# Kernel tuning notes

Hardware: AMD Instinct MI355X
Metric: run time of the kernel (lower is better)

The kernel has to match this reference:

```python
import jax, jax.numpy as jnp
import numpy as np

NUM_HEADS = 16
HEAD_DIM = 128
D = NUM_HEADS * HEAD_DIM  # 2048
B, S = 4, 2048
NEG = jnp.finfo(jnp.float32).min


def setup_inputs() -> dict:
    key = jax.random.key(0)
    ks = jax.random.split(key, 6)
    scale = 1.0 / np.sqrt(D)
    return {
        "hidden_states": jax.random.normal(ks[0], (B, S, D), jnp.float32),
        "wq": jax.random.normal(ks[1], (D, D), jnp.float32) * scale,
        "wk": jax.random.normal(ks[2], (D, D), jnp.float32) * scale,
        "wv": jax.random.normal(ks[3], (D, D), jnp.float32) * scale,
        "wo": jax.random.normal(ks[4], (D, D), jnp.float32) * scale,
        "bo": jnp.zeros((D,), jnp.float32),
    }


def _split_heads(x):
    b, s, _ = x.shape
    return x.reshape(b, s, NUM_HEADS, HEAD_DIM).transpose(0, 2, 1, 3)  # [B,H,S,Dh]


def reference(hidden_states, wq, wk, wv, wo, bo):
    # projections (nn.Linear: x @ W^T), no bias for q/k/v
    q = _split_heads(hidden_states @ wq.T).astype(jnp.float32)
    k = _split_heads(hidden_states @ wk.T).astype(jnp.float32)
    v = _split_heads(hidden_states @ wv.T)
    # GPT-Neo: NO 1/sqrt(d) scaling
    scores = jnp.einsum("bhqd,bhkd->bhqk", q, k)  # [B,H,S,S] fp32
    s = scores.shape[-1]
    causal = jnp.tril(jnp.ones((s, s), bool))  # [S,S]
    scores = jnp.where(causal[None, None], scores, NEG)
    attn_weights = jax.nn.softmax(scores, axis=-1).astype(v.dtype)
    # dropout is identity at eval (p=0.0)
    attn_output = jnp.einsum("bhqk,bhkd->bhqd", attn_weights, v)
    attn_output = attn_output.transpose(0, 2, 1, 3).reshape(hidden_states.shape)
    attn_output = attn_output @ wo.T + bo
    return attn_output, attn_weights
```

## Files before the change

### kernel.cpp

```cpp
#include <hip/hip_runtime.h>

#define DEVFN static __device__ __forceinline__

typedef _Float16 f16;
typedef f16 f16x8 __attribute__((ext_vector_type(8)));
typedef f16 f16x4 __attribute__((ext_vector_type(4)));
typedef float f32x4 __attribute__((ext_vector_type(4)));
typedef short short8 __attribute__((ext_vector_type(8)));

constexpr int Bc = 4, Hn = 16, Sn = 2048, DH = 128, Dn = 2048;
constexpr long MROWS = (long)Bc * Sn;
constexpr long LDQK = 2 * Dn;

template <typename T, typename C>
DEVFN auto mfma_impl(T a, T b, C c, int)
    -> decltype(__builtin_amdgcn_mfma_f32_16x16x32_f16(a, b, c, 0, 0, 0)) {
  return __builtin_amdgcn_mfma_f32_16x16x32_f16(a, b, c, 0, 0, 0);
}
template <typename T, typename C>
DEVFN C mfma_impl(T a, T b, C c, long) {
  return __builtin_amdgcn_mfma_f32_16x16x32_f16(
      __builtin_bit_cast(short8, a), __builtin_bit_cast(short8, b), c, 0, 0, 0);
}
DEVFN f32x4 MFMA(f16x8 a, f16x8 b, f32x4 c) { return mfma_impl(a, b, c, 0); }

DEVFN void nt_store(float* p, float v) { __builtin_nontemporal_store(v, p); }
DEVFN void nt_store4(float* p, f32x4 v) {
  __builtin_nontemporal_store(v, (f32x4*)p);
}

DEVFN void gld_lds16(const f16* g, f16* s) {
  __builtin_amdgcn_global_load_lds(
      (const __attribute__((address_space(1))) unsigned int*)g,
      (__attribute__((address_space(3))) unsigned int*)s, 16, 0, 0);
}

DEVFN void stage_tile(const f16* __restrict__ g, long ld, f16* __restrict__ s) {
  const int t = threadIdx.x;
  const int rr = t >> 3;
  const int cb = (t & 7) * 16;
#pragma unroll
  for (int ch = 0; ch < 4; ++ch) {
    const int r = ch * 32 + rr;
    const int scb = cb ^ ((r & 7) << 4);
    gld_lds16(g + (long)r * ld + (scb >> 1), s + r * 64 + (cb >> 1));
  }
}

DEVFN void stage_tile128(const f16* __restrict__ g, long ld, f16* __restrict__ s) {
  const int t = threadIdx.x;
  const int rr = t >> 4;
  const int cb = (t & 15) * 16;
#pragma unroll
  for (int ch = 0; ch < 8; ++ch) {
    const int r = ch * 16 + rr;
    const int scb = cb ^ ((r & 7) << 4);
    gld_lds16(g + (long)r * ld + (scb >> 1), s + r * 128 + (cb >> 1));
  }
}

DEVFN f16x8 ldfrag(const f16* s, int row, int kelem) {
  const int cb = (kelem * 2) ^ ((row & 7) << 4);
  return *(const f16x8*)(s + row * 64 + (cb >> 1));
}

DEVFN f16x8 ldfrag128(const f16* s, int row, int kelem) {
  const int cb = (kelem * 2) ^ ((row & 7) << 4);
  return *(const f16x8*)((const char*)s + row * 256 + cb);
}

DEVFN f16x8 ldfrag64(const f16* s, int row, int kelem) {
  const int cb = (kelem * 2) ^ ((row & 7) << 4);
  return *(const f16x8*)((const char*)s + row * 128 + cb);
}

__global__ __launch_bounds__(256) void k_cvt_all(
    const float* __restrict__ hid, const float* __restrict__ wq,
    const float* __restrict__ wk, const float* __restrict__ wv,
    const float* __restrict__ wo, f16* __restrict__ h16,
    f16* __restrict__ wqk16, f16* __restrict__ wv16, f16* __restrict__ wo16) {
  const int y = blockIdx.y;
  const long nW = (long)Dn * Dn;
  const float* x;
  f16* out;
  if (y < 4) {
    x = hid + (long)y * nW;
    out = h16 + (long)y * nW;
  } else if (y == 4) {
    x = wq; out = wqk16;
  } else if (y == 5) {
    x = wk; out = wqk16 + nW;
  } else if (y == 6) {
    x = wv; out = wv16;
  } else {
    x = wo; out = wo16;
  }
  const long i = ((long)blockIdx.x * 256 + threadIdx.x) * 4;
  float4 v = *(const float4*)(x + i);
  f16x4 h;
  h[0] = (f16)v.x; h[1] = (f16)v.y; h[2] = (f16)v.z; h[3] = (f16)v.w;
  *(f16x4*)(out + i) = h;
}

DEVFN void gemm_body(const f16* __restrict__ A, long ldA,
                     const f16* __restrict__ B, long ldB, int K,
                     f16* __restrict__ oh, long ldC, int nt, int mt,
                     float oscale, f16* sA, f16* sB) {
  const int tid = threadIdx.x, w = tid >> 6, lane = tid & 63;
  const int wm = (w >> 1) * 64, wn = (w & 1) * 64;
  const int lr = lane & 15, lg = lane >> 4;
  f32x4 acc[4][4] = {};
  const f16* Ab = A + (long)mt * 128 * ldA;
  const f16* Bb = B + (long)nt * 128 * ldB;

  stage_tile(Ab, ldA, sA);
  stage_tile(Bb, ldB, sB);
  __syncthreads();

  int cur = 0;
  for (int kt = 0; kt < K; kt += 64) {
    if (kt + 64 < K) {
      stage_tile(Ab + kt + 64, ldA, sA + (cur ^ 1) * (128 * 64));
      stage_tile(Bb + kt + 64, ldB, sB + (cur ^ 1) * (128 * 64));
    }
    const f16* cA = sA + cur * (128 * 64);
    const f16* cB = sB + cur * (128 * 64);
#pragma unroll
    for (int kk = 0; kk < 64; kk += 32) {
      f16x8 ahf[4], bhf[4];
#pragma unroll
      for (int m = 0; m < 4; ++m) ahf[m] = ldfrag(cA, wm + m * 16 + lr, kk + lg * 8);
#pragma unroll
      for (int n = 0; n < 4; ++n) bhf[n] = ldfrag(cB, wn + n * 16 + lr, kk + lg * 8);
#pragma unroll
      for (int m = 0; m < 4; ++m)
#pragma unroll
        for (int n = 0; n < 4; ++n) acc[m][n] = MFMA(ahf[m], bhf[n], acc[m][n]);
    }
    __syncthreads();
    cur ^= 1;
  }

#pragma unroll
  for (int m = 0; m < 4; ++m)
#pragma unroll
    for (int n = 0; n < 4; ++n) {
      const int col = nt * 128 + wn + n * 16 + lr;
#pragma unroll
      for (int r = 0; r < 4; ++r) {
        const long row = (long)mt * 128 + wm + m * 16 + lg * 4 + r;
        oh[row * ldC + col] = (f16)(acc[m][n][r] * oscale);
      }
    }
}

__global__ __launch_bounds__(256) void k_fused(
    const f16* __restrict__ h16, const f16* __restrict__ wqk16,
    const f16* __restrict__ wv16, f16* __restrict__ qk16, f16* __restrict__ vT) {
  __shared__ __align__(16) f16 sA[2 * 128 * 64];
  __shared__ __align__(16) f16 sB[2 * 128 * 64];
  const int bid = blockIdx.x;
  if (bid < 2048) {
    const int cpx = 2048 >> 3;
    const int swz = (bid & 7) * cpx + (bid >> 3);
    const int nt = swz & 31, mt = swz >> 5;
    const float qsc = (nt < 16) ? 1.44269504f : 1.0f;
    gemm_body(h16, Dn, wqk16, Dn, Dn, qk16, LDQK, nt, mt, qsc, sA, sB);
  } else {
    const int sb = bid - 2048;
    const int cpx = 1024 >> 3;
    const int swz = (sb & 7) * cpx + (sb >> 3);
    const int nt = swz & 63, mt = swz >> 6;
    gemm_body(wv16, Dn, h16, Dn, Dn, vT, MROWS, nt, mt, 1.0f, sA, sB);
  }
}

__global__ __launch_bounds__(256) void k_gemm_wo(
    const f16* __restrict__ A, const f16* __restrict__ B,
    float* __restrict__ of, const float* __restrict__ bias) {
  const int nwgx = gridDim.x;
  const int nwg = nwgx * gridDim.y;
  const int bid = blockIdx.y * nwgx + blockIdx.x;
  const int cpx = nwg >> 3;
  const int swz = (bid & 7) * cpx + (bid >> 3);
  const int nt = swz % nwgx, mt = swz / nwgx;
  __shared__ __align__(16) f16 sA[2][128 * 64];
  __shared__ __align__(16) f16 sB[2][128 * 64];
  const int tid = threadIdx.x, w = tid >> 6, lane = tid & 63;
  const int wm = (w >> 1) * 64, wn = (w & 1) * 64;
  const int lr = lane & 15, lg = lane >> 4;
  f32x4 acc[4][4] = {};
  const f16* Ab = A + (long)mt * 128 * Dn;
  const f16* Bb = B + (long)nt * 128 * Dn;

  stage_tile(Ab, Dn, sA[0]);
  stage_tile(Bb, Dn, sB[0]);
  __syncthreads();

  int cur = 0;
  for (int kt = 0; kt < Dn; kt += 64) {
    if (kt + 64 < Dn) {
      stage_tile(Ab + kt + 64, Dn, sA[cur ^ 1]);
      stage_tile(Bb + kt + 64, Dn, sB[cur ^ 1]);
    }
#pragma unroll
    for (int kk = 0; kk < 64; kk += 32) {
      f16x8 ahf[4], bhf[4];
#pragma unroll
      for (int m = 0; m < 4; ++m) ahf[m] = ldfrag(sA[cur], wm + m * 16 + lr, kk + lg * 8);
#pragma unroll
      for (int n = 0; n < 4; ++n) bhf[n] = ldfrag(sB[cur], wn + n * 16 + lr, kk + lg * 8);
#pragma unroll
      for (int m = 0; m < 4; ++m)
#pragma unroll
        for (int n = 0; n < 4; ++n) acc[m][n] = MFMA(ahf[m], bhf[n], acc[m][n]);
    }
    __syncthreads();
    cur ^= 1;
  }

#pragma unroll
  for (int m = 0; m < 4; ++m)
#pragma unroll
    for (int n = 0; n < 4; ++n) {
      const int col = nt * 128 + wn + n * 16 + lr;
#pragma unroll
      for (int r = 0; r < 4; ++r) {
        const long row = (long)mt * 128 + wm + m * 16 + lg * 4 + r;
        nt_store(of + row * Dn + col, acc[m][n][r] + bias[col]);
      }
    }
}

__global__ __launch_bounds__(256) void k_attn(const f16* __restrict__ qk16,
                                              const f16* __restrict__ vT,
                                              float* __restrict__ wts,
                                              f16* __restrict__ ctx) {
  const int wgid = blockIdx.x;
  const int xcd = wgid & 7, slot = wgid >> 3;
  const int bh = xcd + 8 * (slot >> 4);
  const int qt = 15 - (slot & 15);
  const int b = bh >> 4, h = bh & 15;
  const int tid = threadIdx.x, wv = tid >> 6, lane = tid & 63;
  const int lr = lane & 15, lg = lane >> 4;
  const f16* Qb = qk16 + ((long)b * Sn + qt * 128) * LDQK + h * DH;
  const f16* Kb = qk16 + (long)b * Sn * LDQK + Dn + h * DH;
  const f16* Vb = vT + (long)h * DH * MROWS + (long)b * Sn;
  float* Wrow = wts + (long)bh * Sn * Sn + (long)qt * 128 * Sn;
  __shared__ __align__(16) f16 sK[2][128 * 128];
  __shared__ __align__(16) f16 sQW[128 * 64];

  const int krr = tid >> 4;
  const int kce = (tid & 15) * 8;
  const int kcb = kce * 2;
  f16x8 kpf[8];

#define PRE_K(kt_)                                                              \
  {                                                                             \
    const long kbase = (long)(kt_)*128;                                         \
    _Pragma("unroll") for (int ch = 0; ch < 8; ++ch) kpf[ch] =                  \
        *(const f16x8*)(Kb + (kbase + ch * 16 + krr) * LDQK + kce);             \
  }
#define PUB_K(buf)                                                              \
  {                                                                             \
    _Pragma("unroll") for (int ch = 0; ch < 8; ++ch) {                          \
      const int r = ch * 16 + krr;                                              \
      *(f16x8*)((char*)(buf) + r * 256 + (kcb ^ ((r & 7) << 4))) = kpf[ch];     \
    }                                                                           \
  }

  stage_tile128(Qb, LDQK, sK[0]);
  PRE_K(0);
  __syncthreads();
  const int wq0 = wv * 32;
  f16x8 qf[2][4];
#pragma unroll
  for (int m = 0; m < 2; ++m)
#pragma unroll
    for (int kk = 0; kk < 4; ++kk)
      qf[m][kk] = ldfrag128(sK[0], wq0 + m * 16 + lr, kk * 32 + lg * 8);
  __syncthreads();
  PUB_K(sK[0]);
  if (qt > 0) PRE_K(1);
  __syncthreads();
  int cur = 0;

  float rs[2][4] = {};
  for (int kt = 0; kt <= qt; ++kt) {
    f32x4 acc[2][8] = {};
#pragma unroll
    for (int kk = 0; kk < 4; ++kk) {
      f16x8 bf[8];
#pragma unroll
      for (int n = 0; n < 8; ++n) bf[n] = ldfrag128(sK[cur], n * 16 + lr, kk * 32 + lg * 8);
#pragma unroll
      for (int m = 0; m < 2; ++m)
#pragma unroll
        for (int n = 0; n < 8; ++n) acc[m][n] = MFMA(qf[m][kk], bf[n], acc[m][n]);
    }
    if (kt + 1 <= qt) PUB_K(sK[cur ^ 1]);
    PRE_K(kt + 2 <= qt ? kt + 2 : 0);
    const bool diag = (kt == qt);
#pragma unroll
    for (int m = 0; m < 2; ++m)
#pragma unroll
      for (int r = 0; r < 4; ++r) {
        const int row = wq0 + m * 16 + lg * 4 + r;
        float ts = 0.f;
#pragma unroll
        for (int n = 0; n < 8; ++n) {
          const bool ok = !diag || (n * 16 + lr) <= row;
          ts += ok ? __builtin_amdgcn_exp2f(acc[m][n][r]) : 0.f;
        }
        rs[m][r] += ts;
      }
    __syncthreads();
    cur ^= 1;
  }
  float ri[2][4];
#pragma unroll
  for (int m = 0; m < 2; ++m)
#pragma unroll
    for (int r = 0; r < 4; ++r) {
      float s = rs[m][r];
#pragma unroll
      for (int o = 1; o < 16; o <<= 1) s += __shfl_xor(s, o, 64);
      ri[m][r] = 1.f / s;
    }

  PUB_K(sK[cur ^ 1]);
  if (qt > 0) PRE_K(1);
  __syncthreads();
  cur ^= 1;

  const int ro = lane >> 3, cg = lane & 7;
  f32x4 pacc[2][8] = {};
  for (int kt = 0; kt <= qt; ++kt) {
    f32x4 sacc[2][8] = {};
#pragma unroll
    for (int kk = 0; kk < 4; ++kk) {
      f16x8 bf[8];
#pragma unroll
      for (int n = 0; n < 8; ++n) bf[n] = ldfrag128(sK[cur], n * 16 + lr, kk * 32 + lg * 8);
#pragma unroll
      for (int m = 0; m < 2; ++m)
#pragma unroll
        for (int n = 0; n < 8; ++n) sacc[m][n] = MFMA(qf[m][kk], bf[n], sacc[m][n]);
    }
    if (kt + 1 <= qt) PUB_K(sK[cur ^ 1]);
    if (kt + 2 <= qt) PRE_K(kt + 2);
    const bool diag = (kt == qt);
#pragma unroll
    for (int hf = 0; hf < 2; ++hf) {
#pragma unroll
      for (int m = 0; m < 2; ++m)
#pragma unroll
        for (int n = hf * 4; n < hf * 4 + 4; ++n) {
          const int col = n * 16 + lr;
          const int scol = col - hf * 64;
#pragma unroll
          for (int r = 0; r < 4; ++r) {
            const int row = wq0 + m * 16 + lg * 4 + r;
            float w = __builtin_amdgcn_exp2f(sacc[m][n][r]) * ri[m][r];
            if (diag && col > row) w = 0.f;
            *(f16*)((char*)sQW + row * 128 + ((scol * 2) ^ ((row & 7) << 4))) = (f16)w;
          }
        }
#pragma unroll
      for (int it = 0; it < 4; ++it) {
        const int row = wq0 + it * 8 + ro;
        f16x8 v = ldfrag64(sQW, row, cg * 8);
        f32x4 lo = {(float)v[0], (float)v[1], (float)v[2], (float)v[3]};
        f32x4 hi = {(float)v[4], (float)v[5], (float)v[6], (float)v[7]};
        float* wp = Wrow + (long)row * Sn + kt * 128 + hf * 64 + cg * 8;
        nt_store4(wp, lo);
        nt_store4(wp + 4, hi);
      }
#pragma unroll
      for (int kk = 0; kk < 2; ++kk) {
        f16x8 af[2], bfr[8];
#pragma unroll
        for (int m = 0; m < 2; ++m)
          af[m] = ldfrag64(sQW, wq0 + m * 16 + lr, kk * 32 + lg * 8);
#pragma unroll
        for (int n = 0; n < 8; ++n)
          bfr[n] = *(const f16x8*)(Vb + (long)(n * 16 + lr) * MROWS + kt * 128 + hf * 64 + kk * 32 + lg * 8);
#pragma unroll
        for (int m = 0; m < 2; ++m)
#pragma unroll
          for (int n = 0; n < 8; ++n) pacc[m][n] = MFMA(af[m], bfr[n], pacc[m][n]);
      }
    }
    __syncthreads();
    cur ^= 1;
  }

#pragma unroll
  for (int m = 0; m < 2; ++m)
#pragma unroll
    for (int n = 0; n < 8; ++n) {
      const int d = n * 16 + lr;
#pragma unroll
      for (int r = 0; r < 4; ++r) {
        const int q = qt * 128 + wq0 + m * 16 + lg * 4 + r;
        ctx[(long)(b * Sn + q) * Dn + h * DH + d] = (f16)pacc[m][n][r];
      }
    }

  {
    const int ncols = Sn - (qt + 1) * 128;
    if (ncols > 0) {
      float* base = Wrow + (qt + 1) * 128;
      const f32x4 z = {0.f, 0.f, 0.f, 0.f};
      for (int r = 0; r < 128; ++r) {
        float* rowp = base + (long)r * Sn;
        for (int c = tid * 4; c < ncols; c += 1024) nt_store4(rowp + c, z);
      }
    }
  }
#undef PRE_K
#undef PUB_K
}

extern "C" void kernel_launch(void* const* d_in, const int* in_sizes, int n_in,
                              void* d_out, int out_size, void* d_ws, size_t ws_size,
                              hipStream_t stream) {
  const float* hid = (const float*)d_in[0];
  const float* wq = (const float*)d_in[1];
  const float* wk = (const float*)d_in[2];
  const float* wv = (const float*)d_in[3];
  const float* wo = (const float*)d_in[4];
  const float* bo = (const float*)d_in[5];
  float* out = (float*)d_out;
  float* wts = out + (long)Bc * Sn * Dn;

  char* ws = (char*)d_ws;
  const long MB = 1 << 20;
  f16* h16 = (f16*)(ws + 0 * MB);
  f16* wqk16 = (f16*)(ws + 32 * MB);
  f16* wv16 = (f16*)(ws + 48 * MB);
  f16* wo16 = (f16*)(ws + 56 * MB);
  f16* qk16 = (f16*)(ws + 64 * MB);
  f16* vT = (f16*)(ws + 128 * MB);
  f16* ctx = (f16*)(ws + 160 * MB);

  k_cvt_all<<<dim3(4096, 8), 256, 0, stream>>>(
      hid, wq, wk, wv, wo, h16, wqk16, wv16, wo16);
  k_fused<<<3072, 256, 0, stream>>>(h16, wqk16, wv16, qk16, vT);
  k_attn<<<1024, 256, 0, stream>>>(qk16, vT, wts, ctx);
  k_gemm_wo<<<dim3(16, 64), 256, 0, stream>>>(ctx, wo16, out, bo);
}
```

Measured before the change: 756.6 us.

## Compute transposed scores with 32x32 MFMA and feed P to PV from registers

Switches the attention kernel from 16x16x32 to 32x32x16 MFMA and computes S^T (keys as rows, queries as columns), so each lane owns one query row. The softmax row sum then needs only one cross-lane shuffle. The normalized probabilities are packed to fp16 and exchanged between lane halves to form the B operand of the PV MFMA directly, removing the sQW LDS staging buffer and its round trip. Attention-weight rows are stored straight from registers as float4, which gives a different global store pattern that may coalesce less well.

```diff
diff --git a/kernel.cpp b/kernel.cpp
--- a/kernel.cpp
+++ b/kernel.cpp
@@ -5,7 +5,10 @@
 typedef _Float16 f16;
 typedef f16 f16x8 __attribute__((ext_vector_type(8)));
 typedef f16 f16x4 __attribute__((ext_vector_type(4)));
+typedef f16 f16x2 __attribute__((ext_vector_type(2)));
 typedef float f32x4 __attribute__((ext_vector_type(4)));
+typedef float f32x16 __attribute__((ext_vector_type(16)));
+typedef int i32x4 __attribute__((ext_vector_type(4)));
 typedef short short8 __attribute__((ext_vector_type(8)));
 
 constexpr int Bc = 4, Hn = 16, Sn = 2048, DH = 128, Dn = 2048;
@@ -24,6 +27,18 @@
 }
 DEVFN f32x4 MFMA(f16x8 a, f16x8 b, f32x4 c) { return mfma_impl(a, b, c, 0); }
 
+template <typename T, typename C>
+DEVFN auto mfma32_impl(T a, T b, C c, int)
+    -> decltype(__builtin_amdgcn_mfma_f32_32x32x16_f16(a, b, c, 0, 0, 0)) {
+  return __builtin_amdgcn_mfma_f32_32x32x16_f16(a, b, c, 0, 0, 0);
+}
+template <typename T, typename C>
+DEVFN C mfma32_impl(T a, T b, C c, long) {
+  return __builtin_amdgcn_mfma_f32_32x32x16_f16(
+      __builtin_bit_cast(short8, a), __builtin_bit_cast(short8, b), c, 0, 0, 0);
+}
+DEVFN f32x16 MFMA32(f16x8 a, f16x8 b, f32x16 c) { return mfma32_impl(a, b, c, 0); }
+
 DEVFN void nt_store(float* p, float v) { __builtin_nontemporal_store(v, p); }
 DEVFN void nt_store4(float* p, f32x4 v) {
   __builtin_nontemporal_store(v, (f32x4*)p);
@@ -67,11 +82,6 @@
 DEVFN f16x8 ldfrag128(const f16* s, int row, int kelem) {
   const int cb = (kelem * 2) ^ ((row & 7) << 4);
   return *(const f16x8*)((const char*)s + row * 256 + cb);
-}
-
-DEVFN f16x8 ldfrag64(const f16* s, int row, int kelem) {
-  const int cb = (kelem * 2) ^ ((row & 7) << 4);
-  return *(const f16x8*)((const char*)s + row * 128 + cb);
 }
 
 __global__ __launch_bounds__(256) void k_cvt_all(
@@ -242,13 +252,12 @@
   const int qt = 15 - (slot & 15);
   const int b = bh >> 4, h = bh & 15;
   const int tid = threadIdx.x, wv = tid >> 6, lane = tid & 63;
-  const int lr = lane & 15, lg = lane >> 4;
+  const int l31 = lane & 31, lg1 = lane >> 5;
   const f16* Qb = qk16 + ((long)b * Sn + qt * 128) * LDQK + h * DH;
   const f16* Kb = qk16 + (long)b * Sn * LDQK + Dn + h * DH;
   const f16* Vb = vT + (long)h * DH * MROWS + (long)b * Sn;
   float* Wrow = wts + (long)bh * Sn * Sn + (long)qt * 128 * Sn;
   __shared__ __align__(16) f16 sK[2][128 * 128];
-  __shared__ __align__(16) f16 sQW[128 * 64];
 
   const int krr = tid >> 4;
   const int kce = (tid & 15) * 8;
@@ -273,122 +282,109 @@
   PRE_K(0);
   __syncthreads();
   const int wq0 = wv * 32;
-  f16x8 qf[2][4];
-#pragma unroll
-  for (int m = 0; m < 2; ++m)
-#pragma unroll
-    for (int kk = 0; kk < 4; ++kk)
-      qf[m][kk] = ldfrag128(sK[0], wq0 + m * 16 + lr, kk * 32 + lg * 8);
+  const int qloc = wq0 + l31;
+  f16x8 qf[8];
+#pragma unroll
+  for (int kk = 0; kk < 8; ++kk)
+    qf[kk] = ldfrag128(sK[0], qloc, kk * 16 + lg1 * 8);
   __syncthreads();
   PUB_K(sK[0]);
   if (qt > 0) PRE_K(1);
   __syncthreads();
   int cur = 0;
 
-  float rs[2][4] = {};
+  float rs = 0.f;
   for (int kt = 0; kt <= qt; ++kt) {
-    f32x4 acc[2][8] = {};
-#pragma unroll
-    for (int kk = 0; kk < 4; ++kk) {
-      f16x8 bf[8];
-#pragma unroll
-      for (int n = 0; n < 8; ++n) bf[n] = ldfrag128(sK[cur], n * 16 + lr, kk * 32 + lg * 8);
-#pragma unroll
-      for (int m = 0; m < 2; ++m)
-#pragma unroll
-        for (int n = 0; n < 8; ++n) acc[m][n] = MFMA(qf[m][kk], bf[n], acc[m][n]);
+    f32x16 acc[4] = {};
+#pragma unroll
+    for (int kk = 0; kk < 8; ++kk) {
+      f16x8 kf[4];
+#pragma unroll
+      for (int n = 0; n < 4; ++n)
+        kf[n] = ldfrag128(sK[cur], n * 32 + l31, kk * 16 + lg1 * 8);
+#pragma unroll
+      for (int n = 0; n < 4; ++n) acc[n] = MFMA32(kf[n], qf[kk], acc[n]);
     }
     if (kt + 1 <= qt) PUB_K(sK[cur ^ 1]);
     PRE_K(kt + 2 <= qt ? kt + 2 : 0);
     const bool diag = (kt == qt);
 #pragma unroll
-    for (int m = 0; m < 2; ++m)
-#pragma unroll
-      for (int r = 0; r < 4; ++r) {
-        const int row = wq0 + m * 16 + lg * 4 + r;
-        float ts = 0.f;
-#pragma unroll
-        for (int n = 0; n < 8; ++n) {
-          const bool ok = !diag || (n * 16 + lr) <= row;
-          ts += ok ? __builtin_amdgcn_exp2f(acc[m][n][r]) : 0.f;
-        }
-        rs[m][r] += ts;
+    for (int n = 0; n < 4; ++n)
+#pragma unroll
+      for (int rg = 0; rg < 16; ++rg) {
+        const int keyl = n * 32 + (rg & 3) + 8 * (rg >> 2) + 4 * lg1;
+        const bool ok = !diag || keyl <= qloc;
+        rs += ok ? __builtin_amdgcn_exp2f(acc[n][rg]) : 0.f;
       }
     __syncthreads();
     cur ^= 1;
   }
-  float ri[2][4];
-#pragma unroll
-  for (int m = 0; m < 2; ++m)
-#pragma unroll
-    for (int r = 0; r < 4; ++r) {
-      float s = rs[m][r];
-#pragma unroll
-      for (int o = 1; o < 16; o <<= 1) s += __shfl_xor(s, o, 64);
-      ri[m][r] = 1.f / s;
-    }
+  rs += __shfl_xor(rs, 32, 64);
+  const float ri = 1.f / rs;
 
   PUB_K(sK[cur ^ 1]);
   if (qt > 0) PRE_K(1);
   __syncthreads();
   cur ^= 1;
 
-  const int ro = lane >> 3, cg = lane & 7;
-  f32x4 pacc[2][8] = {};
+  f32x16 pacc[4] = {};
   for (int kt = 0; kt <= qt; ++kt) {
-    f32x4 sacc[2][8] = {};
-#pragma unroll
-    for (int kk = 0; kk < 4; ++kk) {
-      f16x8 bf[8];
-#pragma unroll
-      for (int n = 0; n < 8; ++n) bf[n] = ldfrag128(sK[cur], n * 16 + lr, kk * 32 + lg * 8);
-#pragma unroll
-      for (int m = 0; m < 2; ++m)
-#pragma unroll
-        for (int n = 0; n < 8; ++n) sacc[m][n] = MFMA(qf[m][kk], bf[n], sacc[m][n]);
+    f32x16 sacc[4] = {};
+#pragma unroll
+    for (int kk = 0; kk < 8; ++kk) {
+      f16x8 kf[4];
+#pragma unroll
+      for (int n = 0; n < 4; ++n)
+        kf[n] = ldfrag128(sK[cur], n * 32 + l31, kk * 16 + lg1 * 8);
+#pragma unroll
+      for (int n = 0; n < 4; ++n) sacc[n] = MFMA32(kf[n], qf[kk], sacc[n]);
     }
     if (kt + 1 <= qt) PUB_K(sK[cur ^ 1]);
     if (kt + 2 <= qt) PRE_K(kt + 2);
     const bool diag = (kt == qt);
-#pragma unroll
-    for (int hf = 0; hf < 2; ++hf) {
-#pragma unroll
-      for (int m = 0; m < 2; ++m)
-#pragma unroll
-        for (int n = hf * 4; n < hf * 4 + 4; ++n) {
-          const int col = n * 16 + lr;
-          const int scol = col - hf * 64;
-#pragma unroll
-          for (int r = 0; r < 4; ++r) {
-            const int row = wq0 + m * 16 + lg * 4 + r;
-            float w = __builtin_amdgcn_exp2f(sacc[m][n][r]) * ri[m][r];
-            if (diag && col > row) w = 0.f;
-            *(f16*)((char*)sQW + row * 128 + ((scol * 2) ^ ((row & 7) << 4))) = (f16)w;
-          }
+
+#pragma unroll
+    for (int n = 0; n < 4; ++n) {
+      float w[16];
+#pragma unroll
+      for (int rg = 0; rg < 16; ++rg) {
+        const int keyl = n * 32 + (rg & 3) + 8 * (rg >> 2) + 4 * lg1;
+        float v = __builtin_amdgcn_exp2f(sacc[n][rg]) * ri;
+        if (diag && keyl > qloc) v = 0.f;
+        w[rg] = v;
+      }
+#pragma unroll
+      for (int g = 0; g < 4; ++g) {
+        f32x4 v4 = {w[4 * g], w[4 * g + 1], w[4 * g + 2], w[4 * g + 3]};
+        nt_store4(Wrow + (long)qloc * Sn + kt * 128 + n * 32 + 8 * g + 4 * lg1, v4);
+      }
+#pragma unroll
+      for (int half = 0; half < 2; ++half) {
+        const int kk2 = 2 * n + half;
+        const int g_self = 2 * half + lg1;
+        const int g_send = 2 * half + (1 - lg1);
+        const int d0s = __builtin_bit_cast(
+            int, __builtin_amdgcn_cvt_pkrtz(w[4 * g_self], w[4 * g_self + 1]));
+        const int d1s = __builtin_bit_cast(
+            int, __builtin_amdgcn_cvt_pkrtz(w[4 * g_self + 2], w[4 * g_self + 3]));
+        const int d0x = __builtin_bit_cast(
+            int, __builtin_amdgcn_cvt_pkrtz(w[4 * g_send], w[4 * g_send + 1]));
+        const int d1x = __builtin_bit_cast(
+            int, __builtin_amdgcn_cvt_pkrtz(w[4 * g_send + 2], w[4 * g_send + 3]));
+        const int r0 = __shfl_xor(d0x, 32, 64);
+        const int r1 = __shfl_xor(d1x, 32, 64);
+        i32x4 pk;
+        pk[0] = lg1 ? r0 : d0s;
+        pk[1] = lg1 ? r1 : d1s;
+        pk[2] = lg1 ? d0s : r0;
+        pk[3] = lg1 ? d1s : r1;
+        const f16x8 bp = __builtin_bit_cast(f16x8, pk);
+#pragma unroll
+        for (int nd = 0; nd < 4; ++nd) {
+          const f16x8 av = *(const f16x8*)(
+              Vb + (long)(nd * 32 + l31) * MROWS + kt * 128 + kk2 * 16 + lg1 * 8);
+          pacc[nd] = MFMA32(av, bp, pacc[nd]);
         }
-#pragma unroll
-      for (int it = 0; it < 4; ++it) {
-        const int row = wq0 + it * 8 + ro;
-        f16x8 v = ldfrag64(sQW, row, cg * 8);
-        f32x4 lo = {(float)v[0], (float)v[1], (float)v[2], (float)v[3]};
-        f32x4 hi = {(float)v[4], (float)v[5], (float)v[6], (float)v[7]};
-        float* wp = Wrow + (long)row * Sn + kt * 128 + hf * 64 + cg * 8;
-        nt_store4(wp, lo);
-        nt_store4(wp + 4, hi);
-      }
-#pragma unroll
-      for (int kk = 0; kk < 2; ++kk) {
-        f16x8 af[2], bfr[8];
-#pragma unroll
-        for (int m = 0; m < 2; ++m)
-          af[m] = ldfrag64(sQW, wq0 + m * 16 + lr, kk * 32 + lg * 8);
-#pragma unroll
-        for (int n = 0; n < 8; ++n)
-          bfr[n] = *(const f16x8*)(Vb + (long)(n * 16 + lr) * MROWS + kt * 128 + hf * 64 + kk * 32 + lg * 8);
-#pragma unroll
-        for (int m = 0; m < 2; ++m)
-#pragma unroll
-          for (int n = 0; n < 8; ++n) pacc[m][n] = MFMA(af[m], bfr[n], pacc[m][n]);
       }
     }
     __syncthreads();
@@ -396,15 +392,14 @@
   }
 
 #pragma unroll
-  for (int m = 0; m < 2; ++m)
-#pragma unroll
-    for (int n = 0; n < 8; ++n) {
-      const int d = n * 16 + lr;
-#pragma unroll
-      for (int r = 0; r < 4; ++r) {
-        const int q = qt * 128 + wq0 + m * 16 + lg * 4 + r;
-        ctx[(long)(b * Sn + q) * Dn + h * DH + d] = (f16)pacc[m][n][r];
-      }
+  for (int nd = 0; nd < 4; ++nd)
+#pragma unroll
+    for (int g = 0; g < 4; ++g) {
+      f16x4 t;
+#pragma unroll
+      for (int j = 0; j < 4; ++j) t[j] = (f16)pacc[nd][4 * g + j];
+      const int d = nd * 32 + 8 * g + 4 * lg1;
+      *(f16x4*)(ctx + (long)(b * Sn + qt * 128 + qloc) * Dn + h * DH + d) = t;
     }
 
   {
```

After: 1.122 ms. 48.2% more time.
